# Kernel tuning notes

Measured on AMD Instinct MI355X. Metric: run time of the kernel, lower is better.

## Reference

```python
import jax, jax.numpy as jnp
import numpy as np

D_MODEL = 1024
N_HEADS = 16
D_K = D_MODEL // N_HEADS
D_FF = 4096
EPS = 1e-6


def _layernorm(x, g, b):
    mu = jnp.mean(x, axis=-1, keepdims=True)
    var = jnp.mean(jnp.square(x - mu), axis=-1, keepdims=True)
    return (x - mu) * jax.lax.rsqrt(var + EPS) * g + b


def setup_inputs() -> dict:
    key = jax.random.key(0)
    ks = jax.random.split(key, 12)
    B, S = 2, 2048
    sd_attn = (1.0 / np.sqrt(2.0)) * np.sqrt(2.0 / (D_MODEL + D_MODEL))  # xavier gain 1/sqrt(2) (std approx)
    sd_ff1 = np.sqrt(2.0 / (D_MODEL + D_FF))
    sd_ff2 = np.sqrt(2.0 / (D_FF + D_MODEL))
    return {
        "x": jax.random.normal(ks[0], (B, S, D_MODEL), jnp.float32),
        "mask": jnp.ones((B, S), jnp.int32),
        # weights stored (in, out) so forward is x @ W
        "wq": jax.random.normal(ks[1], (D_MODEL, D_MODEL), jnp.float32) * sd_attn,
        "wk": jax.random.normal(ks[2], (D_MODEL, D_MODEL), jnp.float32) * sd_attn,
        "wv": jax.random.normal(ks[3], (D_MODEL, D_MODEL), jnp.float32) * sd_attn,
        "wo": jax.random.normal(ks[4], (D_MODEL, D_MODEL), jnp.float32) * sd_attn,
        "wo_b": jnp.zeros((D_MODEL,), jnp.float32),
        "w1": jax.random.normal(ks[5], (D_MODEL, D_FF), jnp.float32) * sd_ff1,
        "b1": jnp.zeros((D_FF,), jnp.float32),
        "w2": jax.random.normal(ks[6], (D_FF, D_MODEL), jnp.float32) * sd_ff2,
        "b2": jnp.zeros((D_MODEL,), jnp.float32),
        "g1": jnp.ones((D_MODEL,), jnp.float32),
        "be1": jnp.zeros((D_MODEL,), jnp.float32),
        "g2": jnp.ones((D_MODEL,), jnp.float32),
        "be2": jnp.zeros((D_MODEL,), jnp.float32),
    }


def reference(x, mask, wq, wk, wv, wo, wo_b, w1, b1, w2, b2, g1, be1, g2, be2):
    B, S, _ = x.shape
    scale = 1.0 / np.sqrt(D_K)
    # project and split heads -> [B, H, S, Dk]
    q = (x @ wq).reshape(B, S, N_HEADS, D_K).transpose(0, 2, 1, 3)
    k = (x @ wk).reshape(B, S, N_HEADS, D_K).transpose(0, 2, 1, 3)
    v = (x @ wv).reshape(B, S, N_HEADS, D_K).transpose(0, 2, 1, 3)
    scores = jnp.einsum("bhqd,bhkd->bhqk", q, k) * scale  # [B,H,S,S]
    m = (mask[:, None, None, :] == 0)
    scores = jnp.where(m, -1e9, scores)
    attn = jax.nn.softmax(scores, axis=-1)
    ctx = jnp.einsum("bhqk,bhkd->bhqd", attn, v)
    ctx = ctx.transpose(0, 2, 1, 3).reshape(B, S, D_MODEL)
    attn_out = ctx @ wo + wo_b
    x = _layernorm(x + attn_out, g1, be1)
    ff = jax.nn.gelu(x @ w1 + b1, approximate=False) @ w2 + b2
    return _layernorm(x + ff, g2, be2)
```

## Files before the change

kernel.cpp:

```cpp
#include <hip/hip_runtime.h>
#include <cstdint>

#define DEVINL __device__ __forceinline__

typedef __attribute__((ext_vector_type(8))) short short8;
typedef __attribute__((ext_vector_type(4))) short short4v;
typedef __attribute__((ext_vector_type(4))) float floatx4;
typedef __attribute__((ext_vector_type(4))) unsigned short ushort4v;

DEVINL uint32_t pkbf(float a, float b) {
  uint32_t d;
  asm("v_cvt_pk_bf16_f32 %0, %1, %2" : "=v"(d) : "v"(a), "v"(b));
  return d;
}
DEVINL unsigned short f2bf(float f) {
  union { float f; uint32_t u; } v; v.f = f;
  return (unsigned short)((v.u + 0x7fffu + ((v.u >> 16) & 1u)) >> 16);
}
DEVINL float bf2f(unsigned short h) {
  union { uint32_t u; float f; } v; v.u = ((uint32_t)h) << 16;
  return v.f;
}

#if defined(__has_builtin) && __has_builtin(__builtin_amdgcn_exp2f)
#define EXP2(x) __builtin_amdgcn_exp2f(x)
#else
#define EXP2(x) exp2f(x)
#endif

DEVINL float fast_gelu(float v) {
  const float z = -2.30220795f * v * (1.0f + 0.044715f * v * v);
  return v * __builtin_amdgcn_rcpf(1.0f + EXP2(z));
}

typedef __attribute__((address_space(3))) unsigned char* lds_ptr_t;
typedef const __attribute__((address_space(1))) unsigned char* gbl_ptr_t;
DEVINL void load_lds_128(const void* g, void* l) {
  __builtin_amdgcn_global_load_lds((gbl_ptr_t)g, (lds_ptr_t)l, 16, 0, 0);
}

#define MFMA16(a, b, c) __builtin_amdgcn_mfma_f32_16x16x32_bf16((a), (b), (c), 0, 0, 0)

#define QSCALE2 0.18033688011112042f

__global__ __launch_bounds__(256) void prep_kernel(
    const float* __restrict__ x, unsigned short* __restrict__ XB,
    const float* __restrict__ wq, const float* __restrict__ wk,
    const float* __restrict__ wv, const float* __restrict__ wo,
    unsigned short* __restrict__ WQKV, unsigned short* __restrict__ WOT,
    const float* __restrict__ w1, unsigned short* __restrict__ W1T,
    const float* __restrict__ w2, unsigned short* __restrict__ W2T,
    const int* __restrict__ mask, unsigned short* __restrict__ MB) {
  const int bid = blockIdx.x;
  if (bid >= 16384) {
    const int i0 = threadIdx.x * 16;
#pragma unroll
    for (int j = 0; j < 16; ++j) MB[i0 + j] = mask[i0 + j] ? 0x3F80 : 0;
    return;
  }
  if (bid < 4096) {
    const int i = (bid * 256 + threadIdx.x) * 4;
    floatx4 v = *(const floatx4*)(x + i);
    union { uint32_t u[2]; ushort4v v4; } o;
    o.u[0] = pkbf(v[0], v[1]);
    o.u[1] = pkbf(v[2], v[3]);
    *(ushort4v*)(XB + i) = o.v4;
    return;
  }
  const float* in;
  unsigned short* out;
  int K, N, bx, by;
  if (bid < 8192) {
    const int b2 = bid - 4096, z = b2 >> 10;
    in = (z == 0) ? wq : (z == 1) ? wk : (z == 2) ? wv : wo;
    out = (z == 3) ? WOT : WQKV + (size_t)z * 1024 * 1024;
    K = 1024; N = 1024; bx = b2 & 31; by = (b2 >> 5) & 31;
  } else if (bid < 12288) {
    const int b3 = bid - 8192;
    in = w1; out = W1T; K = 1024; N = 4096; bx = b3 & 127; by = b3 >> 7;
  } else {
    const int b4 = bid - 12288;
    in = w2; out = W2T; K = 4096; N = 1024; bx = b4 & 31; by = b4 >> 5;
  }
  __shared__ float tile[32][33];
  const int n0 = bx * 32, k0 = by * 32;
  const int tx = threadIdx.x & 31, ty = threadIdx.x >> 5;
#pragma unroll
  for (int i = 0; i < 4; ++i)
    tile[ty + 8 * i][tx] = in[(size_t)(k0 + ty + 8 * i) * N + n0 + tx];
  __syncthreads();
#pragma unroll
  for (int i = 0; i < 4; ++i)
    out[(size_t)(n0 + ty + 8 * i) * K + k0 + tx] = f2bf(tile[tx][ty + 8 * i]);
}

template <int EPI, int SK>
__global__ __launch_bounds__(256, 3) void gemm_bt_kernel(
    const unsigned short* __restrict__ A, const unsigned short* __restrict__ BT,
    const float* __restrict__ bias, void* __restrict__ C0, void* __restrict__ C1,
    void* __restrict__ C2, int M, int N, int K, const int* __restrict__ msk) {
  __shared__ __align__(16) unsigned short As[128 * 64];
  __shared__ __align__(16) unsigned short Bs[128 * 64];
  const int tid = threadIdx.x;
  const int w = tid >> 6, l = tid & 63;
  const int lq = l >> 4, lr = l & 15;

  int bxs, bys;
  {
    const int nx = gridDim.x, ny = gridDim.y;
    const int f = blockIdx.y * nx + blockIdx.x;
    const int xcd = f & 7, s = f >> 3;
    const int q = nx >> 1, p = ny >> 2;
    bxs = (xcd & 1) * q + (s % q);
    bys = (xcd >> 1) * p + (s / q);
  }
  const int m0 = bys * 128, n0 = bxs * 128;
  const int wm = (w >> 1) * 64, wn = (w & 1) * 64;
  const int r_a = l >> 2;
  const int colb = (l & 3) * 8;
  const int kslice = K / SK;
  const int kbeg = kslice * blockIdx.z;
  const int region = (EPI == 5) ? (n0 >> 10) : 0;

  uint32_t mbits = 0xFFFFu;
  if (EPI == 5 && region == 2) {
    mbits = 0;
#pragma unroll
    for (int mt = 0; mt < 4; ++mt) {
      const int4 m4 = *(const int4*)(msk + m0 + wm + mt * 16 + lq * 4);
      mbits |= (m4.x ? 1u : 0u) << (mt * 4);
      mbits |= (m4.y ? 1u : 0u) << (mt * 4 + 1);
      mbits |= (m4.z ? 1u : 0u) << (mt * 4 + 2);
      mbits |= (m4.w ? 1u : 0u) << (mt * 4 + 3);
    }
  }

  floatx4 acc[4][4];
  const floatx4 fz = {0.f, 0.f, 0.f, 0.f};
#pragma unroll
  for (int mt = 0; mt < 4; ++mt)
#pragma unroll
    for (int nt = 0; nt < 4; ++nt) acc[mt][nt] = fz;

  for (int k0 = kbeg; k0 < kbeg + kslice; k0 += 64) {
    __syncthreads();
#pragma unroll
    for (int p = 0; p < 2; ++p) {
#pragma unroll
      for (int i = 0; i < 2; ++i) {
        const int c = w * 2 + i;
        load_lds_128(A + (size_t)(m0 + c * 16 + r_a) * K + k0 + p * 32 + colb,
                     (char*)As + p * 8192 + c * 1024);
        load_lds_128(BT + (size_t)(n0 + c * 16 + r_a) * K + k0 + p * 32 + colb,
                     (char*)Bs + p * 8192 + c * 1024);
      }
    }
    __syncthreads();
#pragma unroll
    for (int p = 0; p < 2; ++p) {
      short8 af[4], bf[4];
#pragma unroll
      for (int mt = 0; mt < 4; ++mt)
        af[mt] = *(const short8*)((const char*)As + p * 8192 + (wm + mt * 16 + lr) * 64 + lq * 16);
#pragma unroll
      for (int nt = 0; nt < 4; ++nt)
        bf[nt] = *(const short8*)((const char*)Bs + p * 8192 + (wn + nt * 16 + lr) * 64 + lq * 16);
#pragma unroll
      for (int mt = 0; mt < 4; ++mt)
#pragma unroll
        for (int nt = 0; nt < 4; ++nt)
          acc[mt][nt] = MFMA16(af[mt], bf[nt], acc[mt][nt]);
    }
  }

  void* Cp = (SK > 1 && blockIdx.z) ? C1 : C0;
#pragma unroll
  for (int mt = 0; mt < 4; ++mt) {
#pragma unroll
    for (int nt = 0; nt < 4; ++nt) {
      const int n = n0 + wn + nt * 16 + lr;
      float bval = 0.f;
      if (EPI == 2) bval = bias[n];
#pragma unroll
      for (int r = 0; r < 4; ++r) {
        const int m = m0 + wm + mt * 16 + lq * 4 + r;
        float v = acc[mt][nt][r];
        if (EPI == 4) {
          ((unsigned short*)Cp)[(size_t)m * N + n] = f2bf(v);
        } else if (EPI == 2) {
          ((unsigned short*)C0)[(size_t)m * N + n] = f2bf(fast_gelu(v + bval));
        } else {
          if (region == 0) {
            ((unsigned short*)C0)[(size_t)m * 1024 + n] = f2bf(v * QSCALE2);
          } else if (region == 1) {
            ((unsigned short*)C1)[(size_t)m * 1024 + (n - 1024)] = f2bf(v);
          } else {
            const int nn = n - 2048;
            const int bidx = m >> 11, s = m & 2047;
            const int u = s & 31;
            const int sp = (s & ~31) | (u & 3) | (((u >> 4) & 1) << 2) | (((u >> 2) & 3) << 3);
            const int hh = nn >> 6, d = nn & 63;
            const float vv = ((mbits >> (mt * 4 + r)) & 1u) ? v : 0.f;
            ((unsigned short*)C2)[((size_t)((bidx * 16 + hh) * 64 + d)) * 2048 + sp] = f2bf(vv);
          }
        }
      }
    }
  }
}

__global__ __launch_bounds__(256, 2) void flash_kernel(
    const unsigned short* __restrict__ Q, const unsigned short* __restrict__ Kg,
    const unsigned short* __restrict__ VT, const unsigned short* __restrict__ MB,
    unsigned short* __restrict__ ctx) {
  __shared__ __align__(16) unsigned short Ks[128 * 64];
  __shared__ __align__(16) unsigned short VTs[64 * 128];

  const int tid = threadIdx.x, w = tid >> 6, l = tid & 63;
  const int lq = l >> 4, lr = l & 15;
  const int lin = blockIdx.x;
  const int xcd = lin & 7, slot = lin >> 3;
  const int bh = xcd * 4 + (slot >> 4);
  const int b = bh >> 4, h = bh & 15;
  const int q0 = (slot & 15) * 128;

  const unsigned short* Qp = Q + (size_t)(b * 2048 + q0) * 1024 + h * 64;
  const unsigned short* Kp = Kg + (size_t)(b * 2048) * 1024 + h * 64;
  const unsigned short* VTp = VT + (size_t)bh * 64 * 2048;
  const unsigned short* mbp = MB + b * 2048;

  {
    const int rq = l >> 3, cs = l & 7;
#pragma unroll
    for (int i = 0; i < 4; ++i) {
      const int c = w * 4 + i;
      load_lds_128(Qp + (size_t)(c * 8 + rq) * 1024 + cs * 8, (char*)Ks + c * 1024);
    }
  }
  __syncthreads();
  short8 qf[2][2];
#pragma unroll
  for (int qg = 0; qg < 2; ++qg) {
    qf[qg][0] = *(const short8*)((const char*)Ks + (w * 32 + qg * 16 + lr) * 128 + lq * 16);
    qf[qg][1] = *(const short8*)((const char*)Ks + (w * 32 + qg * 16 + lr) * 128 + 64 + lq * 16);
  }
  __syncthreads();

  const floatx4 fz = {0.f, 0.f, 0.f, 0.f};
  floatx4 o[2][4];
#pragma unroll
  for (int qg = 0; qg < 2; ++qg)
#pragma unroll
    for (int nt = 0; nt < 4; ++nt) o[qg][nt] = fz;
  floatx4 l_acc[2] = {fz, fz};

  const int krow = l >> 3, kslot = l & 7;
  const int vrow = l >> 4, vslot = l & 15;

  for (int kb = 0; kb < 2048; kb += 128) {
    if (kb) __syncthreads();
#pragma unroll
    for (int i = 0; i < 4; ++i) {
      const int c4 = w * 4 + i;
      {
        const int row = c4 * 8 + krow;
        const int cc = kslot ^ (row & 7);
        load_lds_128(Kp + (size_t)(kb + row) * 1024 + cc * 8, (char*)Ks + c4 * 1024);
      }
      {
        const int row = c4 * 4 + vrow;
        const int cc = vslot ^ (row & 15);
        load_lds_128(VTp + (size_t)row * 2048 + kb + cc * 8, (char*)VTs + c4 * 1024);
      }
    }
    short8 mf[4];
#pragma unroll
    for (int t = 0; t < 4; ++t) {
      const short4v ma = *(const short4v*)(mbp + kb + t * 32 + lq * 4);
      const short4v mb2 = *(const short4v*)(mbp + kb + t * 32 + 16 + lq * 4);
      mf[t] = short8{ma[0], ma[1], ma[2], ma[3], mb2[0], mb2[1], mb2[2], mb2[3]};
    }
    __syncthreads();

#pragma unroll
    for (int h2 = 0; h2 < 2; ++h2) {
      floatx4 s[2][4];
#pragma unroll
      for (int gg = 0; gg < 4; ++gg) {
        const int g = h2 * 4 + gg;
        const char* rowp = (const char*)Ks + (g * 16 + lr) * 128;
        short8 k0 = *(const short8*)(rowp + ((lq) ^ (lr & 7)) * 16);
        short8 k1 = *(const short8*)(rowp + ((4 + lq) ^ (lr & 7)) * 16);
#pragma unroll
        for (int qg = 0; qg < 2; ++qg) {
          floatx4 t = MFMA16(k0, qf[qg][0], fz);
          s[qg][gg] = MFMA16(k1, qf[qg][1], t);
        }
      }
      short8 pf[2][2];
#pragma unroll
      for (int qg = 0; qg < 2; ++qg)
#pragma unroll
        for (int tt = 0; tt < 2; ++tt) {
          const floatx4 sL = s[qg][tt * 2], sH = s[qg][tt * 2 + 1];
          union { uint32_t u[4]; short8 s8; } pk;
          pk.u[0] = pkbf(EXP2(sL[0]), EXP2(sL[1]));
          pk.u[1] = pkbf(EXP2(sL[2]), EXP2(sL[3]));
          pk.u[2] = pkbf(EXP2(sH[0]), EXP2(sH[1]));
          pk.u[3] = pkbf(EXP2(sH[2]), EXP2(sH[3]));
          pf[qg][tt] = pk.s8;
        }
#pragma unroll
      for (int tt = 0; tt < 2; ++tt) {
        const int t = h2 * 2 + tt;
        l_acc[0] = MFMA16(pf[0][tt], mf[t], l_acc[0]);
        l_acc[1] = MFMA16(pf[1][tt], mf[t], l_acc[1]);
#pragma unroll
        for (int nt = 0; nt < 4; ++nt) {
          const int d = nt * 16 + lr;
          short8 vf = *(const short8*)((const char*)VTs + d * 256 +
                                       (((t * 4 + lq) ^ (d & 15)) * 16));
          o[0][nt] = MFMA16(pf[0][tt], vf, o[0][nt]);
          o[1][nt] = MFMA16(pf[1][tt], vf, o[1][nt]);
        }
      }
    }
  }

#pragma unroll
  for (int qg = 0; qg < 2; ++qg)
#pragma unroll
    for (int r = 0; r < 4; ++r) {
      const float inv = 1.0f / l_acc[qg][r];
      const int q = q0 + w * 32 + qg * 16 + lq * 4 + r;
#pragma unroll
      for (int nt = 0; nt < 4; ++nt)
        ctx[(size_t)(b * 2048 + q) * 1024 + h * 64 + nt * 16 + lr] = f2bf(o[qg][nt][r] * inv);
    }
}

template <int RESBF, int OUTBF>
__global__ __launch_bounds__(256) void ln2_kernel(
    const void* __restrict__ res, const unsigned short* __restrict__ y0,
    const unsigned short* __restrict__ y1, const float* __restrict__ bias,
    const float* __restrict__ gamma, const float* __restrict__ beta,
    void* __restrict__ outp) {
  const int row = blockIdx.x, t = threadIdx.x;
  const size_t base = (size_t)row * 1024 + t * 4;
  float v[4];
  if (RESBF) {
    ushort4v r4 = *(const ushort4v*)((const unsigned short*)res + base);
#pragma unroll
    for (int j = 0; j < 4; ++j) v[j] = bf2f(r4[j]);
  } else {
    floatx4 r4 = *(const floatx4*)((const float*)res + base);
#pragma unroll
    for (int j = 0; j < 4; ++j) v[j] = r4[j];
  }
  const ushort4v a4 = *(const ushort4v*)(y0 + base);
  const ushort4v b4v = *(const ushort4v*)(y1 + base);
  const floatx4 bi4 = *(const floatx4*)(bias + t * 4);
  float s = 0.f, ss = 0.f;
#pragma unroll
  for (int j = 0; j < 4; ++j) {
    v[j] += bf2f(a4[j]) + bf2f(b4v[j]) + bi4[j];
    s += v[j];
    ss += v[j] * v[j];
  }
#pragma unroll
  for (int off = 1; off < 64; off <<= 1) {
    s += __shfl_xor(s, off);
    ss += __shfl_xor(ss, off);
  }
  __shared__ float red[8];
  const int w = t >> 6;
  if ((t & 63) == 0) { red[w] = s; red[4 + w] = ss; }
  __syncthreads();
  s = red[0] + red[1] + red[2] + red[3];
  ss = red[4] + red[5] + red[6] + red[7];
  const float mean = s * (1.0f / 1024.0f);
  const float var = ss * (1.0f / 1024.0f) - mean * mean;
  const float rstd = rsqrtf(var + 1e-6f);
  const floatx4 g4 = *(const floatx4*)(gamma + t * 4);
  const floatx4 be4 = *(const floatx4*)(beta + t * 4);
  if (OUTBF) {
    union { uint32_t u[2]; ushort4v v4; } o;
    o.u[0] = pkbf((v[0] - mean) * rstd * g4[0] + be4[0],
                  (v[1] - mean) * rstd * g4[1] + be4[1]);
    o.u[1] = pkbf((v[2] - mean) * rstd * g4[2] + be4[2],
                  (v[3] - mean) * rstd * g4[3] + be4[3]);
    *(ushort4v*)((unsigned short*)outp + base) = o.v4;
  } else {
    floatx4 o;
#pragma unroll
    for (int j = 0; j < 4; ++j) o[j] = (v[j] - mean) * rstd * g4[j] + be4[j];
    *(floatx4*)((float*)outp + base) = o;
  }
}

extern "C" void kernel_launch(void* const* d_in, const int* in_sizes, int n_in,
                              void* d_out, int out_size, void* d_ws, size_t ws_size,
                              hipStream_t stream) {
  (void)in_sizes; (void)n_in; (void)out_size; (void)ws_size;
  const float* x    = (const float*)d_in[0];
  const int*   mask = (const int*)d_in[1];
  const float* wq   = (const float*)d_in[2];
  const float* wk   = (const float*)d_in[3];
  const float* wv   = (const float*)d_in[4];
  const float* wo   = (const float*)d_in[5];
  const float* wo_b = (const float*)d_in[6];
  const float* w1   = (const float*)d_in[7];
  const float* b1   = (const float*)d_in[8];
  const float* w2   = (const float*)d_in[9];
  const float* b2   = (const float*)d_in[10];
  const float* g1   = (const float*)d_in[11];
  const float* be1  = (const float*)d_in[12];
  const float* g2   = (const float*)d_in[13];
  const float* be2  = (const float*)d_in[14];
  float* out = (float*)d_out;

  char* ws = (char*)d_ws;
  const size_t MBy = 1024ull * 1024ull;
  unsigned short* WQKV = (unsigned short*)(ws + 0 * MBy);
  unsigned short* WOT  = (unsigned short*)(ws + 6 * MBy);
  unsigned short* W1T  = (unsigned short*)(ws + 8 * MBy);
  unsigned short* W2T  = (unsigned short*)(ws + 16 * MBy);
  unsigned short* XB   = (unsigned short*)(ws + 24 * MBy);
  unsigned short* Qb   = (unsigned short*)(ws + 32 * MBy);
  unsigned short* Kb   = (unsigned short*)(ws + 40 * MBy);
  unsigned short* VTb  = (unsigned short*)(ws + 48 * MBy);
  unsigned short* CTX  = (unsigned short*)(ws + 56 * MBy);
  unsigned short* ATT0 = (unsigned short*)(ws + 32 * MBy);
  unsigned short* ATT1 = (unsigned short*)(ws + 40 * MBy);
  unsigned short* Hb   = (unsigned short*)(ws + 24 * MBy);
  unsigned short* G1   = (unsigned short*)(ws + 32 * MBy);
  unsigned short* FF20 = (unsigned short*)(ws + 64 * MBy);
  unsigned short* FF21 = (unsigned short*)(ws + 72 * MBy);
  unsigned short* MB   = (unsigned short*)(ws + 78 * MBy);

  prep_kernel<<<16385, 256, 0, stream>>>(x, XB, wq, wk, wv, wo, WQKV, WOT,
                                         w1, W1T, w2, W2T, mask, MB);
  gemm_bt_kernel<5, 1><<<dim3(24, 32), 256, 0, stream>>>(
      XB, WQKV, nullptr, Qb, Kb, VTb, 4096, 3072, 1024, mask);
  flash_kernel<<<512, 256, 0, stream>>>(Qb, Kb, VTb, MB, CTX);
  gemm_bt_kernel<4, 2><<<dim3(8, 32, 2), 256, 0, stream>>>(
      CTX, WOT, nullptr, ATT0, ATT1, nullptr, 4096, 1024, 1024, nullptr);
  ln2_kernel<0, 1><<<4096, 256, 0, stream>>>(x, ATT0, ATT1, wo_b, g1, be1, Hb);
  gemm_bt_kernel<2, 1><<<dim3(32, 32), 256, 0, stream>>>(
      Hb, W1T, b1, G1, nullptr, nullptr, 4096, 4096, 1024, nullptr);
  gemm_bt_kernel<4, 2><<<dim3(8, 32, 2), 256, 0, stream>>>(
      G1, W2T, nullptr, FF20, FF21, nullptr, 4096, 1024, 4096, nullptr);
  ln2_kernel<1, 0><<<4096, 256, 0, stream>>>(Hb, FF20, FF21, b2, g2, be2, out);
}
```

Measured before the change: 330.0 us.

## Add 256x256-tile 8-wave GEMM with double-buffered LDS for QKV and FFN

Adds a new GEMM kernel with 512 threads and a 256x256 output tile. It double-buffers 128KB of XOR-swizzled LDS, interleaves prefetch with MFMA phases, and raises wave priority during the MFMA sections. The kernel replaces the 128x128 GEMM for the QKV projection, FFN1 and FFN2, and FFN2 now uses a 4-way split-K whose partials are summed in the LayerNorm kernel. The aim is more data reuse per LDS load and better overlap of memory and compute. In exchange it gets fewer blocks (low occupancy on 256 CUs), more split-K partial traffic, and reuses workspace regions for the partials.

```diff
diff --git a/kernel.cpp b/kernel.cpp
--- a/kernel.cpp
+++ b/kernel.cpp
@@ -120,20 +120,6 @@
   const int colb = (l & 3) * 8;
   const int kslice = K / SK;
   const int kbeg = kslice * blockIdx.z;
-  const int region = (EPI == 5) ? (n0 >> 10) : 0;
-
-  uint32_t mbits = 0xFFFFu;
-  if (EPI == 5 && region == 2) {
-    mbits = 0;
-#pragma unroll
-    for (int mt = 0; mt < 4; ++mt) {
-      const int4 m4 = *(const int4*)(msk + m0 + wm + mt * 16 + lq * 4);
-      mbits |= (m4.x ? 1u : 0u) << (mt * 4);
-      mbits |= (m4.y ? 1u : 0u) << (mt * 4 + 1);
-      mbits |= (m4.z ? 1u : 0u) << (mt * 4 + 2);
-      mbits |= (m4.w ? 1u : 0u) << (mt * 4 + 3);
-    }
-  }
 
   floatx4 acc[4][4];
   const floatx4 fz = {0.f, 0.f, 0.f, 0.f};
@@ -184,6 +170,188 @@
 #pragma unroll
       for (int r = 0; r < 4; ++r) {
         const int m = m0 + wm + mt * 16 + lq * 4 + r;
+        float v = acc[mt][nt][r];
+        if (EPI == 4) {
+          ((unsigned short*)Cp)[(size_t)m * N + n] = f2bf(v);
+        } else if (EPI == 2) {
+          ((unsigned short*)C0)[(size_t)m * N + n] = f2bf(fast_gelu(v + bval));
+        }
+      }
+    }
+  }
+  (void)msk; (void)C2; (void)M;
+}
+
+template <int EPI, int SK>
+__global__ __launch_bounds__(512, 2) void gemm8_kernel(
+    const unsigned short* __restrict__ A, const unsigned short* __restrict__ BT,
+    const float* __restrict__ bias, void* __restrict__ C0, void* __restrict__ C1,
+    void* __restrict__ C2, void* __restrict__ C3, int M, int N, int K,
+    const int* __restrict__ msk) {
+  __shared__ __align__(16) char smem[131072];
+  const int tid = threadIdx.x;
+  const int w = tid >> 6, l = tid & 63;
+  const int lq = l >> 4, lr = l & 15;
+  const int wr = w >> 2, wc = w & 3;
+
+  int bxs, bys;
+  {
+    const int nx = gridDim.x, ny = gridDim.y;
+    const int f = blockIdx.y * nx + blockIdx.x;
+    const int xcd = f & 7, s = f >> 3;
+    const int q = nx >> 1, p = ny >> 2;
+    bxs = (xcd & 1) * q + (s % q);
+    bys = (xcd >> 1) * p + (s / q);
+  }
+  const int m0 = bys * 256, n0 = bxs * 256;
+  const int kslice = K / SK;
+  const int kbeg = kslice * blockIdx.z;
+  const int NT = kslice >> 6;
+  const int region = (EPI == 5) ? (n0 >> 10) : 0;
+
+  uint32_t mbits = 0xFFFFFFFFu;
+  if (EPI == 5 && region == 2) {
+    mbits = 0;
+#pragma unroll
+    for (int mt = 0; mt < 8; ++mt) {
+      const int4 m4 = *(const int4*)(msk + m0 + wr * 128 + mt * 16 + lq * 4);
+      mbits |= (m4.x ? 1u : 0u) << (mt * 4);
+      mbits |= (m4.y ? 1u : 0u) << (mt * 4 + 1);
+      mbits |= (m4.z ? 1u : 0u) << (mt * 4 + 2);
+      mbits |= (m4.w ? 1u : 0u) << (mt * 4 + 3);
+    }
+  }
+
+  const int awb = w << 10;
+  const int bwb = ((w >> 2) << 13) | ((w & 3) << 10);
+
+  auto stage = [&](const unsigned short* __restrict__ G, int row0, int k,
+                   int toff, int wb) {
+    const int a = wb + (l << 4);
+    const int r = a >> 7;
+    const int cb = (a & 127) ^ ((r & 7) << 4);
+    load_lds_128(G + (size_t)(row0 + r) * K + k + (cb >> 1), smem + toff + wb);
+  };
+  auto stgAX = [&](int co, int k) { stage(A, m0, k, co, awb); stage(A, m0, k, co, 16384 + awb); };
+  auto stgAY = [&](int co, int k) { stage(A, m0, k, co, 8192 + awb); stage(A, m0, k, co, 24576 + awb); };
+  auto stgBX = [&](int co, int k) { stage(BT, n0, k, co + 32768, bwb); stage(BT, n0, k, co + 32768, 16384 + bwb); };
+  auto stgBY = [&](int co, int k) { stage(BT, n0, k, co + 32768, 4096 + bwb); stage(BT, n0, k, co + 32768, 20480 + bwb); };
+
+  floatx4 acc[8][4];
+  const floatx4 fz = {0.f, 0.f, 0.f, 0.f};
+#pragma unroll
+  for (int mt = 0; mt < 8; ++mt)
+#pragma unroll
+    for (int nt = 0; nt < 4; ++nt) acc[mt][nt] = fz;
+
+  stgAX(0, kbeg); stgAY(0, kbeg); stgBX(0, kbeg); stgBY(0, kbeg);
+  stgAX(65536, kbeg + 64); stgAY(65536, kbeg + 64);
+  stgBX(65536, kbeg + 64); stgBY(65536, kbeg + 64);
+  asm volatile("s_waitcnt vmcnt(8)" ::: "memory");
+  __builtin_amdgcn_s_barrier();
+
+  const int arow = wr * 16384 + lr * 128;
+  const int brow = wc * 8192 + lr * 128;
+  const int xr = (lr & 7) << 4;
+  const int cb0 = (lq * 16) ^ xr;
+  const int cb1 = (64 + lq * 16) ^ xr;
+
+  for (int t = 0; t < NT; ++t) {
+    const int co = (t & 1) << 16;
+    const char* Ab = (const char*)smem + co;
+    const char* Bb = (const char*)smem + co + 32768;
+    const int kpre = kbeg + (t + 2) * 64;
+    const bool pre = (t + 2) < NT;
+    short8 af[4][2], bX[2][2], bY[2][2];
+
+#pragma unroll
+    for (int mt = 0; mt < 4; ++mt) {
+      af[mt][0] = *(const short8*)(Ab + arow + mt * 2048 + cb0);
+      af[mt][1] = *(const short8*)(Ab + arow + mt * 2048 + cb1);
+    }
+#pragma unroll
+    for (int nt = 0; nt < 2; ++nt) {
+      bX[nt][0] = *(const short8*)(Bb + brow + nt * 2048 + cb0);
+      bX[nt][1] = *(const short8*)(Bb + brow + nt * 2048 + cb1);
+    }
+    __builtin_amdgcn_s_barrier();
+    __builtin_amdgcn_s_setprio(1);
+#pragma unroll
+    for (int mt = 0; mt < 4; ++mt)
+#pragma unroll
+      for (int nt = 0; nt < 2; ++nt) {
+        acc[mt][nt] = MFMA16(af[mt][0], bX[nt][0], acc[mt][nt]);
+        acc[mt][nt] = MFMA16(af[mt][1], bX[nt][1], acc[mt][nt]);
+      }
+    __builtin_amdgcn_s_setprio(0);
+    __builtin_amdgcn_s_barrier();
+
+#pragma unroll
+    for (int nt = 0; nt < 2; ++nt) {
+      bY[nt][0] = *(const short8*)(Bb + brow + (2 + nt) * 2048 + cb0);
+      bY[nt][1] = *(const short8*)(Bb + brow + (2 + nt) * 2048 + cb1);
+    }
+    if (pre) { stgAX(co, kpre); stgBX(co, kpre); }
+    __builtin_amdgcn_s_barrier();
+    __builtin_amdgcn_s_setprio(1);
+#pragma unroll
+    for (int mt = 0; mt < 4; ++mt)
+#pragma unroll
+      for (int nt = 0; nt < 2; ++nt) {
+        acc[mt][2 + nt] = MFMA16(af[mt][0], bY[nt][0], acc[mt][2 + nt]);
+        acc[mt][2 + nt] = MFMA16(af[mt][1], bY[nt][1], acc[mt][2 + nt]);
+      }
+    __builtin_amdgcn_s_setprio(0);
+    __builtin_amdgcn_s_barrier();
+
+#pragma unroll
+    for (int mt = 0; mt < 4; ++mt) {
+      af[mt][0] = *(const short8*)(Ab + arow + (4 + mt) * 2048 + cb0);
+      af[mt][1] = *(const short8*)(Ab + arow + (4 + mt) * 2048 + cb1);
+    }
+    if (pre) stgBY(co, kpre);
+    __builtin_amdgcn_s_barrier();
+    __builtin_amdgcn_s_setprio(1);
+#pragma unroll
+    for (int mt = 0; mt < 4; ++mt)
+#pragma unroll
+      for (int nt = 0; nt < 2; ++nt) {
+        acc[4 + mt][2 + nt] = MFMA16(af[mt][0], bY[nt][0], acc[4 + mt][2 + nt]);
+        acc[4 + mt][2 + nt] = MFMA16(af[mt][1], bY[nt][1], acc[4 + mt][2 + nt]);
+      }
+    __builtin_amdgcn_s_setprio(0);
+    __builtin_amdgcn_s_barrier();
+
+    if (pre) stgAY(co, kpre);
+    __builtin_amdgcn_s_barrier();
+    __builtin_amdgcn_s_setprio(1);
+#pragma unroll
+    for (int mt = 0; mt < 4; ++mt)
+#pragma unroll
+      for (int nt = 0; nt < 2; ++nt) {
+        acc[4 + mt][nt] = MFMA16(af[mt][0], bX[nt][0], acc[4 + mt][nt]);
+        acc[4 + mt][nt] = MFMA16(af[mt][1], bX[nt][1], acc[4 + mt][nt]);
+      }
+    __builtin_amdgcn_s_setprio(0);
+    asm volatile("s_waitcnt vmcnt(8)" ::: "memory");
+    __builtin_amdgcn_s_barrier();
+  }
+
+  void* Cp = C0;
+  if (EPI == 4 && SK > 1) {
+    const int z = blockIdx.z;
+    Cp = (z == 0) ? C0 : (z == 1) ? C1 : (z == 2) ? C2 : C3;
+  }
+#pragma unroll
+  for (int mt = 0; mt < 8; ++mt) {
+#pragma unroll
+    for (int nt = 0; nt < 4; ++nt) {
+      const int n = n0 + wc * 64 + nt * 16 + lr;
+      float bval = 0.f;
+      if (EPI == 2) bval = bias[n];
+#pragma unroll
+      for (int r = 0; r < 4; ++r) {
+        const int m = m0 + wr * 128 + mt * 16 + lq * 4 + r;
         float v = acc[mt][nt][r];
         if (EPI == 4) {
           ((unsigned short*)Cp)[(size_t)m * N + n] = f2bf(v);
@@ -207,6 +375,7 @@
       }
     }
   }
+  (void)M;
 }
 
 __global__ __launch_bounds__(256, 2) void flash_kernel(
@@ -339,10 +508,11 @@
     }
 }
 
-template <int RESBF, int OUTBF>
+template <int RESBF, int OUTBF, int NY>
 __global__ __launch_bounds__(256) void ln2_kernel(
     const void* __restrict__ res, const unsigned short* __restrict__ y0,
-    const unsigned short* __restrict__ y1, const float* __restrict__ bias,
+    const unsigned short* __restrict__ y1, const unsigned short* __restrict__ y2,
+    const unsigned short* __restrict__ y3, const float* __restrict__ bias,
     const float* __restrict__ gamma, const float* __restrict__ beta,
     void* __restrict__ outp) {
   const int row = blockIdx.x, t = threadIdx.x;
@@ -359,11 +529,17 @@
   }
   const ushort4v a4 = *(const ushort4v*)(y0 + base);
   const ushort4v b4v = *(const ushort4v*)(y1 + base);
+  ushort4v c4 = {0, 0, 0, 0}, d4 = {0, 0, 0, 0};
+  if (NY == 4) {
+    c4 = *(const ushort4v*)(y2 + base);
+    d4 = *(const ushort4v*)(y3 + base);
+  }
   const floatx4 bi4 = *(const floatx4*)(bias + t * 4);
   float s = 0.f, ss = 0.f;
 #pragma unroll
   for (int j = 0; j < 4; ++j) {
     v[j] += bf2f(a4[j]) + bf2f(b4v[j]) + bi4[j];
+    if (NY == 4) v[j] += bf2f(c4[j]) + bf2f(d4[j]);
     s += v[j];
     ss += v[j] * v[j];
   }
@@ -434,21 +610,24 @@
   unsigned short* ATT1 = (unsigned short*)(ws + 40 * MBy);
   unsigned short* Hb   = (unsigned short*)(ws + 24 * MBy);
   unsigned short* G1   = (unsigned short*)(ws + 32 * MBy);
-  unsigned short* FF20 = (unsigned short*)(ws + 64 * MBy);
-  unsigned short* FF21 = (unsigned short*)(ws + 72 * MBy);
+  unsigned short* P0   = (unsigned short*)(ws + 0 * MBy);
+  unsigned short* P1   = (unsigned short*)(ws + 8 * MBy);
+  unsigned short* P2   = (unsigned short*)(ws + 64 * MBy);
+  unsigned short* P3   = (unsigned short*)(ws + 72 * MBy);
   unsigned short* MB   = (unsigned short*)(ws + 78 * MBy);
 
   prep_kernel<<<16385, 256, 0, stream>>>(x, XB, wq, wk, wv, wo, WQKV, WOT,
                                          w1, W1T, w2, W2T, mask, MB);
-  gemm_bt_kernel<5, 1><<<dim3(24, 32), 256, 0, stream>>>(
-      XB, WQKV, nullptr, Qb, Kb, VTb, 4096, 3072, 1024, mask);
+  gemm8_kernel<5, 1><<<dim3(12, 16), 512, 0, stream>>>(
+      XB, WQKV, nullptr, Qb, Kb, VTb, nullptr, 4096, 3072, 1024, mask);
   flash_kernel<<<512, 256, 0, stream>>>(Qb, Kb, VTb, MB, CTX);
   gemm_bt_kernel<4, 2><<<dim3(8, 32, 2), 256, 0, stream>>>(
       CTX, WOT, nullptr, ATT0, ATT1, nullptr, 4096, 1024, 1024, nullptr);
-  ln2_kernel<0, 1><<<4096, 256, 0, stream>>>(x, ATT0, ATT1, wo_b, g1, be1, Hb);
-  gemm_bt_kernel<2, 1><<<dim3(32, 32), 256, 0, stream>>>(
-      Hb, W1T, b1, G1, nullptr, nullptr, 4096, 4096, 1024, nullptr);
-  gemm_bt_kernel<4, 2><<<dim3(8, 32, 2), 256, 0, stream>>>(
-      G1, W2T, nullptr, FF20, FF21, nullptr, 4096, 1024, 4096, nullptr);
-  ln2_kernel<1, 0><<<4096, 256, 0, stream>>>(Hb, FF20, FF21, b2, g2, be2, out);
-}
+  ln2_kernel<0, 1, 2><<<4096, 256, 0, stream>>>(x, ATT0, ATT1, nullptr, nullptr,
+                                                wo_b, g1, be1, Hb);
+  gemm8_kernel<2, 1><<<dim3(16, 16), 512, 0, stream>>>(
+      Hb, W1T, b1, G1, nullptr, nullptr, nullptr, 4096, 4096, 1024, nullptr);
+  gemm8_kernel<4, 4><<<dim3(4, 16, 4), 512, 0, stream>>>(
+      G1, W2T, nullptr, P0, P1, P2, P3, 4096, 1024, 4096, nullptr);
+  ln2_kernel<1, 0, 4><<<4096, 256, 0, stream>>>(Hb, P0, P1, P2, P3, b2, g2, be2, out);
+}
```

Result: no change. 333.1 us (+1.0%).
